# Performance work log

Measured on AMD Instinct MI355X. Metric: run time of the kernel, lower is better.

Reference implementation:

```python
import jax, jax.numpy as jnp
import numpy as np

HIDDEN_DIM = 1024
NUM_EXPERTS = 8
BASE_LR = 0.5
LR_DECAY = 0.85
TOLERANCE = 0.001


def setup_inputs() -> dict:
    key = jax.random.key(0)
    ks = jax.random.split(key, 8)
    B, T, D, E = 4, 2048, HIDDEN_DIM, NUM_EXPERTS
    x_real = jax.random.normal(ks[0], (B, T, D), dtype=jnp.float32)
    x_imag = jax.random.normal(ks[1], (B, T, D), dtype=jnp.float32)
    phase_offset = jax.random.uniform(ks[2], (D,), dtype=jnp.float32) * 2.0 * np.pi
    Wg = jax.random.normal(ks[3], (D, E), dtype=jnp.float32) / np.sqrt(D)
    bg = jnp.zeros((E,), dtype=jnp.float32)
    We = jax.random.normal(ks[4], (E, D, D), dtype=jnp.float32) / np.sqrt(D)
    be = jnp.zeros((E, D), dtype=jnp.float32)
    return {"x_real": x_real, "x_imag": x_imag, "phase_offset": phase_offset,
            "Wg": Wg, "bg": bg, "We": We, "be": be, "local_iterations": 8}


def _moe(z, Wg, bg, We, be, capacity):
    # z: [N, D] complex64. Expert-choice routing on the real part.
    N, D = z.shape
    logits = z.real @ Wg + bg                     # [N, E]
    S = jax.nn.softmax(logits, axis=-1)           # [N, E]
    scores, idx = jax.lax.top_k(S.T, capacity)    # each [E, k]
    gathered = z[idx]                             # [E, k, D] complex
    out_e = jnp.einsum('ekd,edh->ekh', gathered, We.astype(z.dtype)) + be[:, None, :]
    y = jnp.zeros((N, D), z.dtype).at[idx.reshape(-1)].add(
        (scores[..., None] * out_e).reshape(-1, D))
    return y


def _build_target(z, phase_offset):
    # z: [B, T, D] complex; target[t] = z[t-1] * exp(i*phase), target[0] = z[0]
    rot = jnp.exp(1j * phase_offset)              # [D] complex64
    return jnp.concatenate([z[:, :1, :], z[:, :-1, :] * rot], axis=1)


def reference(x_real, x_imag, phase_offset, Wg, bg, We, be, local_iterations):
    B, T, D = x_real.shape
    N = B * T
    capacity = N // NUM_EXPERTS
    z0 = (x_real + 1j * x_imag).astype(jnp.complex64)  # [B, T, D]
    target = _build_target(z0, phase_offset)
    max_iters = max(1, int(local_iterations) - 1)

    def cond(carry):
        it, z, lr, done = carry
        return jnp.logical_and(it < max_iters, jnp.logical_not(done))

    def body(carry):
        it, z, lr, _ = carry
        pred = _moe(z.reshape(N, D), Wg, bg, We, be, capacity).reshape(B, T, D)
        residual = target - pred
        z = z + lr.astype(z.dtype) * residual
        res_mean = jnp.mean(jnp.abs(residual))
        return (it + 1, z, lr * LR_DECAY, res_mean < TOLERANCE)

    it0 = jnp.array(0, jnp.int32)
    lr0 = jnp.array(BASE_LR, jnp.float32)
    iters_run, z_final, _, _ = jax.lax.while_loop(cond, body, (it0, z0, lr0, jnp.array(False)))

    target_grad = _build_target(z0, phase_offset)
    pred_grad = _moe(z_final.reshape(N, D), Wg, bg, We, be, capacity).reshape(B, T, D)
    out = z_final + BASE_LR * (target_grad - pred_grad)   # [B, T, D] complex
    out_stacked = jnp.stack([out.real, out.imag], axis=-1)  # [B, T, D, 2] float32
    return out_stacked, iters_run
```

## Files before the change

kernel.cpp:

```cpp
#include <hip/hip_runtime.h>
#include <math.h>

#define ND    8388608
#define NTOK  8192
#define DIM   1024
#define NEXP  8
#define CAP   1024
#define TSEQ  2048

typedef short bf16x8 __attribute__((ext_vector_type(8)));
typedef unsigned short u16x8 __attribute__((ext_vector_type(8)));
typedef float f32x4 __attribute__((ext_vector_type(4)));

#define AS1 __attribute__((address_space(1)))
#define AS3 __attribute__((address_space(3)))

__device__ __forceinline__ void gload_lds16(const void* g, void* l) {
    __builtin_amdgcn_global_load_lds((const AS1 unsigned int*)g,
                                     (AS3 unsigned int*)l, 16, 0, 0);
}

__device__ __forceinline__ unsigned short f2bf(float x) {
    union { float f; unsigned u; } v; v.f = x;
    unsigned r = v.u + 0x7FFFu + ((v.u >> 16) & 1u);
    return (unsigned short)(r >> 16);
}
__device__ __forceinline__ float bf2f(unsigned short b) {
    union { unsigned u; float f; } v; v.u = ((unsigned)b) << 16; return v.f;
}

__global__ void k_init_small(const float* __restrict__ phase, const int* __restrict__ Lptr,
                             float* __restrict__ rc, float* __restrict__ rs,
                             int* __restrict__ ctl) {
    int d = blockIdx.x * blockDim.x + threadIdx.x;
    if (d < DIM) { rc[d] = cosf(phase[d]); rs[d] = sinf(phase[d]); }
    if (d == 0) {
        ctl[0] = 0; ctl[1] = 0;
        int L = Lptr[0]; int mi = L - 1; if (mi < 1) mi = 1;
        ctl[2] = mi;
    }
}

__global__ void k_init_big(const float* __restrict__ xr, const float* __restrict__ xi,
                           float* __restrict__ zre, unsigned short* __restrict__ zimB) {
    int i = blockIdx.x * blockDim.x + threadIdx.x;
    if (i >= ND) return;
    zre[i] = xr[i];
    zimB[i] = f2bf(xi[i]);
}

__global__ __launch_bounds__(256) void k_wconv(const float* __restrict__ We,
                                               unsigned short* __restrict__ Whi,
                                               unsigned short* __restrict__ Wlo) {
    __shared__ float lds[64][65];
    int e = blockIdx.z, h0 = blockIdx.x * 64, d0 = blockIdx.y * 64;
    int tid = threadIdx.x;
    #pragma unroll
    for (int q = 0; q < 16; ++q) {
        int idx = q * 256 + tid;
        int i = idx >> 6, j = idx & 63;
        lds[i][j] = We[(size_t)e * 1048576 + (size_t)(d0 + i) * 1024 + h0 + j];
    }
    __syncthreads();
    #pragma unroll
    for (int q = 0; q < 2; ++q) {
        int sid = q * 256 + tid;
        int j = sid >> 3, sp = sid & 7;
        int h = h0 + j;
        int slog = sp ^ (h & 7);
        u16x8 hi, lo;
        #pragma unroll
        for (int u = 0; u < 8; ++u) {
            float x = lds[slog * 8 + u][j];
            unsigned short hb = f2bf(x);
            hi[u] = hb;
            lo[u] = f2bf(x - bf2f(hb));
        }
        size_t o = (((size_t)(e << 10) + h) << 10) + d0 + sp * 8;
        *(u16x8*)(Whi + o) = hi;
        *(u16x8*)(Wlo + o) = lo;
    }
}

__global__ __launch_bounds__(256) void k_gate(
    const float* __restrict__ zre, const float* __restrict__ Wg, const float* __restrict__ bg,
    float* __restrict__ S, int* __restrict__ tokcnt,
    const int* __restrict__ ctl, int iter) {
    if (iter >= 0 && (ctl[0] || iter >= ctl[2])) return;
    const int w = threadIdx.x >> 6, lane = threadIdx.x & 63;
    const int n = blockIdx.x * 4 + w;
    const float* zr = zre + ((size_t)n << 10);
    float acc[8] = {0,0,0,0,0,0,0,0};
    #pragma unroll
    for (int q = 0; q < 4; ++q) {
        const int d0 = q * 256 + lane * 4;
        float4 zv = *(const float4*)(zr + d0);
        float zz[4] = {zv.x, zv.y, zv.z, zv.w};
        #pragma unroll
        for (int j = 0; j < 4; ++j) {
            const float4 w0 = *(const float4*)(Wg + (d0 + j) * 8);
            const float4 w1 = *(const float4*)(Wg + (d0 + j) * 8 + 4);
            acc[0] += zz[j] * w0.x; acc[1] += zz[j] * w0.y; acc[2] += zz[j] * w0.z; acc[3] += zz[j] * w0.w;
            acc[4] += zz[j] * w1.x; acc[5] += zz[j] * w1.y; acc[6] += zz[j] * w1.z; acc[7] += zz[j] * w1.w;
        }
    }
    #pragma unroll
    for (int off = 32; off > 0; off >>= 1)
        #pragma unroll
        for (int e = 0; e < 8; ++e) acc[e] += __shfl_xor(acc[e], off);
    if (lane == 0) {
        float m = -1e30f;
        #pragma unroll
        for (int e = 0; e < 8; ++e) { acc[e] += bg[e]; m = fmaxf(m, acc[e]); }
        float sum = 0.f;
        #pragma unroll
        for (int e = 0; e < 8; ++e) { acc[e] = expf(acc[e] - m); sum += acc[e]; }
        float inv = 1.0f / sum;
        *(float4*)(S + (n << 3))     = (float4){acc[0]*inv, acc[1]*inv, acc[2]*inv, acc[3]*inv};
        *(float4*)(S + (n << 3) + 4) = (float4){acc[4]*inv, acc[5]*inv, acc[6]*inv, acc[7]*inv};
        tokcnt[n] = 0;
    }
}

__global__ __launch_bounds__(1024) void k_route(
    const float* __restrict__ S, int* __restrict__ idxs, int* __restrict__ tokcnt,
    int* __restrict__ ent_id, const int* __restrict__ ctl, int iter) {
    if (iter >= 0 && (ctl[0] || iter >= ctl[2])) return;
    __shared__ unsigned keys[NTOK];
    __shared__ unsigned hA[2048];
    __shared__ unsigned hB[2048];
    __shared__ int sbkt, srem, sntie, scnt;
    const int e = blockIdx.x, tid = threadIdx.x;
    if (tid == 0) scnt = 0;
    for (int n = tid; n < NTOK; n += 1024) keys[n] = __float_as_uint(S[(n << 3) + e]);
    __syncthreads();

    int rem = CAP;
    unsigned pref = 0;
    #pragma unroll
    for (int lvl = 0; lvl < 3; ++lvl) {
        const int nb = (lvl == 2) ? 1024 : 2048;
        for (int i = tid; i < nb; i += 1024) hA[i] = 0;
        __syncthreads();
        for (int n = tid; n < NTOK; n += 1024) {
            unsigned k = keys[n];
            bool ok; unsigned b;
            if (lvl == 0)      { ok = true;                 b = k >> 21; }
            else if (lvl == 1) { ok = (k >> 21) == pref;    b = (k >> 10) & 2047u; }
            else               { ok = (k >> 10) == pref;    b = k & 1023u; }
            if (ok) atomicAdd(&hA[b], 1u);
        }
        __syncthreads();
        unsigned* src = hA; unsigned* dst = hB;
        for (int off = 1; off < nb; off <<= 1) {
            for (int i = tid; i < nb; i += 1024)
                dst[i] = src[i] + ((i + off < nb) ? src[i + off] : 0u);
            __syncthreads();
            unsigned* t = src; src = dst; dst = t;
        }
        for (int i = tid; i < nb; i += 1024) {
            unsigned sfi = src[i];
            unsigned sfn = (i + 1 < nb) ? src[i + 1] : 0u;
            if (sfi >= (unsigned)rem && sfn < (unsigned)rem) {
                sbkt = i; srem = rem - (int)sfn; sntie = (int)(sfi - sfn);
            }
        }
        __syncthreads();
        int b = sbkt; rem = srem;
        if (lvl == 0)      pref = (unsigned)b;
        else if (lvl == 1) pref = (pref << 11) | (unsigned)b;
        else               pref = (pref << 10) | (unsigned)b;
        __syncthreads();
    }
    const unsigned T = pref;
    const int remv = rem;
    const bool allt = (remv == sntie);

    for (int n = tid; n < NTOK; n += 1024) {
        unsigned k = keys[n];
        bool sel = (k > T);
        if (k == T) {
            if (allt) sel = true;
            else {
                int r = 0;
                int j = 0;
                for (; j + 8 <= n; j += 8) {
                    r += (int)(keys[j] == T) + (int)(keys[j+1] == T) + (int)(keys[j+2] == T)
                       + (int)(keys[j+3] == T) + (int)(keys[j+4] == T) + (int)(keys[j+5] == T)
                       + (int)(keys[j+6] == T) + (int)(keys[j+7] == T);
                }
                for (; j < n; ++j) r += (int)(keys[j] == T);
                sel = (r < remv);
            }
        }
        if (sel) {
            int slot = atomicAdd(&scnt, 1);
            int row = (e << 10) + slot;
            idxs[row] = n;
            int p = atomicAdd(&tokcnt[n], 1);
            ent_id[(n << 3) + p] = row;
        }
    }
}

__global__ __launch_bounds__(256, 2) void k_gemm_cx(
    const float* __restrict__ zre, const unsigned short* __restrict__ zimB,
    const unsigned short* __restrict__ Whi, const unsigned short* __restrict__ Wlo,
    const float* __restrict__ be, const int* __restrict__ idxs,
    float* __restrict__ outre, float* __restrict__ outim,
    const int* __restrict__ ctl, int iter) {
    if (iter >= 0 && (ctl[0] || iter >= ctl[2])) return;
    extern __shared__ unsigned short smem[];
    const int bid = blockIdx.x;
    const int e = bid & 7, bx = (bid >> 3) & 7, by = bid >> 6;
    const int tid = threadIdx.x;
    const int wid = tid >> 6, lane = tid & 63;
    const int wm = wid >> 1, wn = wid & 1;

    const unsigned short* gsrc = nullptr;
    unsigned short* ldst = nullptr;
    if (wid >= 2) {
        const unsigned short* wsb = (wid == 2) ? Whi : Wlo;
        int rowbase = (e << 10) + bx * 128;
        gsrc = wsb + (((size_t)(rowbase + (lane >> 3))) << 10) + ((lane & 7) << 3);
        ldst = smem + ((wid == 2) ? 24576 : 32768);
    }

    const int rl = lane >> 3;
    const int ch = lane & 7;
    const int slog8 = (ch ^ rl) << 3;
    int tok[4];
    #pragma unroll
    for (int q = 0; q < 4; ++q)
        tok[q] = idxs[(e << 10) + by * 128 + (wid << 5) + (q << 3) + rl];

    f32x4 accre[4][4], accim[4][4];
    #pragma unroll
    for (int a = 0; a < 4; ++a)
        #pragma unroll
        for (int b = 0; b < 4; ++b) {
            accre[a][b] = (f32x4){0.f, 0.f, 0.f, 0.f};
            accim[a][b] = (f32x4){0.f, 0.f, 0.f, 0.f};
        }

    for (int kt = 0; kt < DIM; kt += 64) {
        if (kt) __syncthreads();
        if (wid >= 2) {
            #pragma unroll
            for (int i = 0; i < 16; ++i)
                gload_lds16(gsrc + kt + ((size_t)i << 13), ldst + i * 512);
        }
        float4 a0[4], a1[4]; u16x8 im[4];
        #pragma unroll
        for (int q = 0; q < 4; ++q) {
            const float* zsrc = zre + ((size_t)tok[q] << 10) + kt + slog8;
            a0[q] = *(const float4*)zsrc;
            a1[q] = *(const float4*)(zsrc + 4);
            im[q] = *(const u16x8*)(zimB + ((size_t)tok[q] << 10) + kt + slog8);
        }
        #pragma unroll
        for (int q = 0; q < 4; ++q) {
            const int r = (wid << 5) + (q << 3) + rl;
            const int lo_off = (r << 6) + (ch << 3);
            float xv[8] = {a0[q].x, a0[q].y, a0[q].z, a0[q].w,
                           a1[q].x, a1[q].y, a1[q].z, a1[q].w};
            u16x8 hi, lo;
            #pragma unroll
            for (int u = 0; u < 8; ++u) {
                unsigned short hb = f2bf(xv[u]);
                hi[u] = hb;
                lo[u] = f2bf(xv[u] - bf2f(hb));
            }
            *(u16x8*)&smem[lo_off]         = hi;
            *(u16x8*)&smem[8192 + lo_off]  = lo;
            *(u16x8*)&smem[16384 + lo_off] = im[q];
        }
        __syncthreads();
        #pragma unroll
        for (int ks = 0; ks < 2; ++ks) {
            const int slog = (ks << 2) + (lane >> 4);
            const int swz = (slog ^ (lane & 7)) << 3;
            bf16x8 ah[4], al[4], am[4], bh[4], bl[4];
            #pragma unroll
            for (int mi = 0; mi < 4; ++mi) {
                int off = ((wm * 64 + mi * 16 + (lane & 15)) << 6) + swz;
                ah[mi] = *(const bf16x8*)&smem[off];
                al[mi] = *(const bf16x8*)&smem[8192 + off];
                am[mi] = *(const bf16x8*)&smem[16384 + off];
            }
            #pragma unroll
            for (int ni = 0; ni < 4; ++ni) {
                int off = ((wn * 64 + ni * 16 + (lane & 15)) << 6) + swz;
                bh[ni] = *(const bf16x8*)&smem[24576 + off];
                bl[ni] = *(const bf16x8*)&smem[32768 + off];
            }
            #pragma unroll
            for (int mi = 0; mi < 4; ++mi)
                #pragma unroll
                for (int ni = 0; ni < 4; ++ni) {
                    accre[mi][ni] = __builtin_amdgcn_mfma_f32_16x16x32_bf16(ah[mi], bh[ni], accre[mi][ni], 0, 0, 0);
                    accre[mi][ni] = __builtin_amdgcn_mfma_f32_16x16x32_bf16(ah[mi], bl[ni], accre[mi][ni], 0, 0, 0);
                    accre[mi][ni] = __builtin_amdgcn_mfma_f32_16x16x32_bf16(al[mi], bh[ni], accre[mi][ni], 0, 0, 0);
                    accim[mi][ni] = __builtin_amdgcn_mfma_f32_16x16x32_bf16(am[mi], bh[ni], accim[mi][ni], 0, 0, 0);
                }
        }
    }
    const int colbase = bx * 128 + wn * 64 + (lane & 15);
    float bev[4];
    #pragma unroll
    for (int ni = 0; ni < 4; ++ni) bev[ni] = be[(e << 10) + colbase + ni * 16];
    const int rowloc = by * 128 + wm * 64 + ((lane >> 4) << 2);
    float* obr = outre + (((size_t)(e << 10) + rowloc) << 10) + colbase;
    float* obi = outim + (((size_t)(e << 10) + rowloc) << 10) + colbase;
    #pragma unroll
    for (int mi = 0; mi < 4; ++mi)
        #pragma unroll
        for (int rg = 0; rg < 4; ++rg) {
            size_t ro = (size_t)(mi * 16 + rg) << 10;
            #pragma unroll
            for (int ni = 0; ni < 4; ++ni) {
                obr[ro + ni * 16] = accre[mi][ni][rg] + bev[ni];
                obi[ro + ni * 16] = accim[mi][ni][rg];
            }
        }
}

__global__ __launch_bounds__(256) void k_resid_gate(
    float* __restrict__ zre, unsigned short* __restrict__ zimB,
    const float* __restrict__ xr, const float* __restrict__ xi,
    const float* __restrict__ rc, const float* __restrict__ rs,
    const float* __restrict__ outre, const float* __restrict__ outim,
    int* __restrict__ tokcnt, const int* __restrict__ ent_id,
    float* __restrict__ S, const float* __restrict__ Wg, const float* __restrict__ bg,
    float lr, float* __restrict__ partial, const int* __restrict__ ctl, int iter) {
    if (ctl[0] || iter >= ctl[2]) return;
    __shared__ float wred[4][8];
    const int n = blockIdx.x;
    const int tid = threadIdx.x;
    const int d0 = tid << 2;
    const int kc = tokcnt[n];
    const int4 e0 = *(const int4*)(ent_id + (n << 3));
    const int4 e1 = *(const int4*)(ent_id + (n << 3) + 4);
    const int rows[8] = {e0.x, e0.y, e0.z, e0.w, e1.x, e1.y, e1.z, e1.w};

    float pr[4] = {0,0,0,0}, pm[4] = {0,0,0,0};
    #pragma unroll
    for (int k = 0; k < 8; ++k) {
        if (k < kc) {
            const int row = rows[k];
            const float s = S[(n << 3) + (row >> 10)];
            const float4 vr = *(const float4*)(outre + ((size_t)row << 10) + d0);
            const float4 vi = *(const float4*)(outim + ((size_t)row << 10) + d0);
            pr[0] += s * vr.x; pr[1] += s * vr.y; pr[2] += s * vr.z; pr[3] += s * vr.w;
            pm[0] += s * vi.x; pm[1] += s * vi.y; pm[2] += s * vi.z; pm[3] += s * vi.w;
        }
    }
    const size_t base = ((size_t)n << 10) + d0;
    const int t = n & (TSEQ - 1);
    float tr[4], ti[4];
    if (t == 0) {
        float4 a = *(const float4*)(xr + base), b = *(const float4*)(xi + base);
        tr[0]=a.x; tr[1]=a.y; tr[2]=a.z; tr[3]=a.w;
        ti[0]=b.x; ti[1]=b.y; ti[2]=b.z; ti[3]=b.w;
    } else {
        float4 a = *(const float4*)(xr + base - DIM), b = *(const float4*)(xi + base - DIM);
        float4 c = *(const float4*)(rc + d0), s4 = *(const float4*)(rs + d0);
        tr[0]=a.x*c.x-b.x*s4.x; tr[1]=a.y*c.y-b.y*s4.y; tr[2]=a.z*c.z-b.z*s4.z; tr[3]=a.w*c.w-b.w*s4.w;
        ti[0]=a.x*s4.x+b.x*c.x; ti[1]=a.y*s4.y+b.y*c.y; ti[2]=a.z*s4.z+b.z*c.z; ti[3]=a.w*s4.w+b.w*c.w;
    }
    float4 zr4 = *(const float4*)(zre + base);
    ushort4 zi4 = *(const ushort4*)(zimB + base);
    float zrv[4] = {zr4.x, zr4.y, zr4.z, zr4.w};
    unsigned short ziv[4] = {zi4.x, zi4.y, zi4.z, zi4.w};
    float zn[4]; unsigned short zo[4];
    float lsum = 0.f;
    float lac[8] = {0,0,0,0,0,0,0,0};
    #pragma unroll
    for (int j = 0; j < 4; ++j) {
        float rr = tr[j] - pr[j];
        float ri = ti[j] - pm[j];
        zn[j] = zrv[j] + lr * rr;
        zo[j] = f2bf(bf2f(ziv[j]) + lr * ri);
        lsum += sqrtf(rr * rr + ri * ri);
        const float4 w0 = *(const float4*)(Wg + (d0 + j) * 8);
        const float4 w1 = *(const float4*)(Wg + (d0 + j) * 8 + 4);
        lac[0] += zn[j] * w0.x; lac[1] += zn[j] * w0.y; lac[2] += zn[j] * w0.z; lac[3] += zn[j] * w0.w;
        lac[4] += zn[j] * w1.x; lac[5] += zn[j] * w1.y; lac[6] += zn[j] * w1.z; lac[7] += zn[j] * w1.w;
    }
    *(float4*)(zre + base) = (float4){zn[0], zn[1], zn[2], zn[3]};
    *(ushort4*)(zimB + base) = (ushort4){zo[0], zo[1], zo[2], zo[3]};

    const int w = tid >> 6, lane = tid & 63;
    #pragma unroll
    for (int off = 32; off > 0; off >>= 1) {
        lsum += __shfl_xor(lsum, off);
        #pragma unroll
        for (int e = 0; e < 8; ++e) lac[e] += __shfl_xor(lac[e], off);
    }
    if (lane == 0) {
        #pragma unroll
        for (int e = 0; e < 8; ++e) wred[w][e] = lac[e];
        partial[(n << 2) + w] = lsum;
    }
    __syncthreads();
    if (tid == 0) {
        float lg[8];
        float m = -1e30f;
        #pragma unroll
        for (int e = 0; e < 8; ++e) {
            lg[e] = wred[0][e] + wred[1][e] + wred[2][e] + wred[3][e] + bg[e];
            m = fmaxf(m, lg[e]);
        }
        float sum = 0.f;
        #pragma unroll
        for (int e = 0; e < 8; ++e) { lg[e] = expf(lg[e] - m); sum += lg[e]; }
        float inv = 1.0f / sum;
        *(float4*)(S + (n << 3))     = (float4){lg[0]*inv, lg[1]*inv, lg[2]*inv, lg[3]*inv};
        *(float4*)(S + (n << 3) + 4) = (float4){lg[4]*inv, lg[5]*inv, lg[6]*inv, lg[7]*inv};
        tokcnt[n] = 0;
    }
}

__global__ __launch_bounds__(1024) void k_finalize(
    const float* __restrict__ partial, int* __restrict__ ctl, int iter) {
    if (ctl[0] || iter >= ctl[2]) return;
    __shared__ float red[16];
    float s = 0.f;
    for (int i = threadIdx.x; i < NTOK * 4; i += 1024) s += partial[i];
    #pragma unroll
    for (int off = 32; off > 0; off >>= 1) s += __shfl_xor(s, off);
    if ((threadIdx.x & 63) == 0) red[threadIdx.x >> 6] = s;
    __syncthreads();
    if (threadIdx.x == 0) {
        float tot = 0.f;
        #pragma unroll
        for (int w = 0; w < 16; ++w) tot += red[w];
        ctl[1] = iter + 1;
        if (tot * (1.0f / (float)ND) < 0.001f) ctl[0] = 1;
    }
}

__global__ __launch_bounds__(256) void k_final_zupd(
    float* __restrict__ zre, unsigned short* __restrict__ zimB,
    const float* __restrict__ xr, const float* __restrict__ xi,
    const float* __restrict__ rc, const float* __restrict__ rs,
    const float* __restrict__ outre, const float* __restrict__ outim,
    const int* __restrict__ tokcnt, const int* __restrict__ ent_id,
    const float* __restrict__ S) {
    const int n = blockIdx.x;
    const int tid = threadIdx.x;
    const int d0 = tid << 2;
    const int kc = tokcnt[n];
    const int4 e0 = *(const int4*)(ent_id + (n << 3));
    const int4 e1 = *(const int4*)(ent_id + (n << 3) + 4);
    const int rows[8] = {e0.x, e0.y, e0.z, e0.w, e1.x, e1.y, e1.z, e1.w};
    float pr[4] = {0,0,0,0}, pm[4] = {0,0,0,0};
    #pragma unroll
    for (int k = 0; k < 8; ++k) {
        if (k < kc) {
            const int row = rows[k];
            const float s = S[(n << 3) + (row >> 10)];
            const float4 vr = *(const float4*)(outre + ((size_t)row << 10) + d0);
            const float4 vi = *(const float4*)(outim + ((size_t)row << 10) + d0);
            pr[0] += s * vr.x; pr[1] += s * vr.y; pr[2] += s * vr.z; pr[3] += s * vr.w;
            pm[0] += s * vi.x; pm[1] += s * vi.y; pm[2] += s * vi.z; pm[3] += s * vi.w;
        }
    }
    const size_t base = ((size_t)n << 10) + d0;
    const int t = n & (TSEQ - 1);
    float tr[4], ti[4];
    if (t == 0) {
        float4 a = *(const float4*)(xr + base), b = *(const float4*)(xi + base);
        tr[0]=a.x; tr[1]=a.y; tr[2]=a.z; tr[3]=a.w;
        ti[0]=b.x; ti[1]=b.y; ti[2]=b.z; ti[3]=b.w;
    } else {
        float4 a = *(const float4*)(xr + base - DIM), b = *(const float4*)(xi + base - DIM);
        float4 c = *(const float4*)(rc + d0), s4 = *(const float4*)(rs + d0);
        tr[0]=a.x*c.x-b.x*s4.x; tr[1]=a.y*c.y-b.y*s4.y; tr[2]=a.z*c.z-b.z*s4.z; tr[3]=a.w*c.w-b.w*s4.w;
        ti[0]=a.x*s4.x+b.x*c.x; ti[1]=a.y*s4.y+b.y*c.y; ti[2]=a.z*s4.z+b.z*c.z; ti[3]=a.w*s4.w+b.w*c.w;
    }
    float4 zr4 = *(const float4*)(zre + base);
    ushort4 zi4 = *(const ushort4*)(zimB + base);
    float zrv[4] = {zr4.x, zr4.y, zr4.z, zr4.w};
    unsigned short ziv[4] = {zi4.x, zi4.y, zi4.z, zi4.w};
    float zn[4]; unsigned short zo[4];
    #pragma unroll
    for (int j = 0; j < 4; ++j) {
        zn[j] = zrv[j] + 0.5f * (tr[j] - pr[j]);
        zo[j] = f2bf(bf2f(ziv[j]) + 0.5f * (ti[j] - pm[j]));
    }
    *(float4*)(zre + base) = (float4){zn[0], zn[1], zn[2], zn[3]};
    *(ushort4*)(zimB + base) = (ushort4){zo[0], zo[1], zo[2], zo[3]};
}

__global__ void k_write_out(const float* __restrict__ zre, const unsigned short* __restrict__ zimB,
                            float* __restrict__ out, const int* __restrict__ ctl) {
    int i = blockIdx.x * blockDim.x + threadIdx.x;
    if (i >= ND) return;
    out[2 * i]     = zre[i];
    out[2 * i + 1] = bf2f(zimB[i]);
    if (i == 0) out[(size_t)2 * ND] = (float)ctl[1];
}

extern "C" void kernel_launch(void* const* d_in, const int* in_sizes, int n_in,
                              void* d_out, int out_size, void* d_ws, size_t ws_size,
                              hipStream_t stream) {
    (void)in_sizes; (void)n_in; (void)out_size; (void)ws_size;
    const float* x_real = (const float*)d_in[0];
    const float* x_imag = (const float*)d_in[1];
    const float* phase  = (const float*)d_in[2];
    const float* Wg     = (const float*)d_in[3];
    const float* bg     = (const float*)d_in[4];
    const float* We     = (const float*)d_in[5];
    const float* be     = (const float*)d_in[6];
    const int*   Lptr   = (const int*)d_in[7];

    char* wsb = (char*)d_ws;
    float*          zre  = (float*)wsb;
    unsigned short* zimB = (unsigned short*)(wsb + 33554432);
    unsigned short* Whi  = (unsigned short*)(wsb + 50331648);
    unsigned short* Wlo  = (unsigned short*)(wsb + 67108864);
    float*    S       = (float*)(wsb + 83886080);
    int*      ent_id  = (int*)  (wsb + 84148224);
    int*      idxs    = (int*)  (wsb + 84410368);
    int*      tokcnt  = (int*)  (wsb + 84443136);
    float*    partial = (float*)(wsb + 84475904);
    float*    rc      = (float*)(wsb + 84606976);
    float*    rs      = (float*)(wsb + 84611072);
    int*      ctl     = (int*)  (wsb + 84615168);

    float* outre = (float*)d_out;
    float* outim = outre + (size_t)ND;

    k_init_small<<<4, 256, 0, stream>>>(phase, Lptr, rc, rs, ctl);
    k_init_big<<<ND / 256, 256, 0, stream>>>(x_real, x_imag, zre, zimB);
    k_wconv<<<dim3(16, 16, 8), 256, 0, stream>>>(We, Whi, Wlo);
    k_gate<<<NTOK / 4, 256, 0, stream>>>(zre, Wg, bg, S, tokcnt, ctl, -1);

    const size_t gemm_lds = 40960 * sizeof(unsigned short);
    float lr = 0.5f;
    for (int it = 0; it < 7; ++it) {
        k_route<<<NEXP, 1024, 0, stream>>>(S, idxs, tokcnt, ent_id, ctl, it);
        k_gemm_cx<<<512, 256, gemm_lds, stream>>>(zre, zimB, Whi, Wlo, be, idxs,
                                                  outre, outim, ctl, it);
        k_resid_gate<<<NTOK, 256, 0, stream>>>(zre, zimB, x_real, x_imag, rc, rs,
                                               outre, outim, tokcnt, ent_id, S, Wg, bg,
                                               lr, partial, ctl, it);
        k_finalize<<<1, 1024, 0, stream>>>(partial, ctl, it);
        lr *= 0.85f;
    }

    k_route<<<NEXP, 1024, 0, stream>>>(S, idxs, tokcnt, ent_id, ctl, -1);
    k_gemm_cx<<<512, 256, gemm_lds, stream>>>(zre, zimB, Whi, Wlo, be, idxs,
                                              outre, outim, ctl, -1);
    k_final_zupd<<<NTOK, 256, 0, stream>>>(zre, zimB, x_real, x_imag, rc, rs,
                                           outre, outim, tokcnt, ent_id, S);
    k_write_out<<<ND / 256, 256, 0, stream>>>(zre, zimB, (float*)d_out, ctl);
}
```

Before: 1.239 ms.

## Store real state as split bf16 hi/lo planes and DMA gathered rows into LDS

The real part of z is now stored as two bf16 planes (hi and lo) instead of fp32, and the split is done by the producer kernels (init, residual update) rather than inside the GEMM. The GEMM then gathers token rows straight into LDS with global_load_lds from three warps, while the fourth warp and partial slices handle the weight tiles. This drops the per-tile fp32 load, convert and LDS store from the GEMM inner loop, and merges init_big into the gate kernel. In exchange, every z update re-splits into hi/lo and the real state keeps only about bf16+bf16 precision, so rounding can drift slightly across iterations.

After: 1.160 ms. -6.4%, faster.

```diff
diff --git a/kernel.cpp b/kernel.cpp
--- a/kernel.cpp
+++ b/kernel.cpp
@@ -41,14 +41,6 @@
     }
 }
 
-__global__ void k_init_big(const float* __restrict__ xr, const float* __restrict__ xi,
-                           float* __restrict__ zre, unsigned short* __restrict__ zimB) {
-    int i = blockIdx.x * blockDim.x + threadIdx.x;
-    if (i >= ND) return;
-    zre[i] = xr[i];
-    zimB[i] = f2bf(xi[i]);
-}
-
 __global__ __launch_bounds__(256) void k_wconv(const float* __restrict__ We,
                                                unsigned short* __restrict__ Whi,
                                                unsigned short* __restrict__ Wlo) {
@@ -82,27 +74,38 @@
     }
 }
 
-__global__ __launch_bounds__(256) void k_gate(
-    const float* __restrict__ zre, const float* __restrict__ Wg, const float* __restrict__ bg,
-    float* __restrict__ S, int* __restrict__ tokcnt,
-    const int* __restrict__ ctl, int iter) {
-    if (iter >= 0 && (ctl[0] || iter >= ctl[2])) return;
+__global__ __launch_bounds__(256) void k_init_gate(
+    const float* __restrict__ xr, const float* __restrict__ xi,
+    unsigned short* __restrict__ zhi, unsigned short* __restrict__ zlo,
+    unsigned short* __restrict__ zimB,
+    const float* __restrict__ Wg, const float* __restrict__ bg,
+    float* __restrict__ S, int* __restrict__ tokcnt) {
     const int w = threadIdx.x >> 6, lane = threadIdx.x & 63;
     const int n = blockIdx.x * 4 + w;
-    const float* zr = zre + ((size_t)n << 10);
     float acc[8] = {0,0,0,0,0,0,0,0};
     #pragma unroll
     for (int q = 0; q < 4; ++q) {
         const int d0 = q * 256 + lane * 4;
-        float4 zv = *(const float4*)(zr + d0);
-        float zz[4] = {zv.x, zv.y, zv.z, zv.w};
+        const size_t base = ((size_t)n << 10) + d0;
+        float4 xv = *(const float4*)(xr + base);
+        float4 iv = *(const float4*)(xi + base);
+        float zz[4] = {xv.x, xv.y, xv.z, xv.w};
+        float zi[4] = {iv.x, iv.y, iv.z, iv.w};
+        unsigned short h4[4], l4[4], i4[4];
         #pragma unroll
         for (int j = 0; j < 4; ++j) {
+            unsigned short hb = f2bf(zz[j]);
+            h4[j] = hb;
+            l4[j] = f2bf(zz[j] - bf2f(hb));
+            i4[j] = f2bf(zi[j]);
             const float4 w0 = *(const float4*)(Wg + (d0 + j) * 8);
             const float4 w1 = *(const float4*)(Wg + (d0 + j) * 8 + 4);
             acc[0] += zz[j] * w0.x; acc[1] += zz[j] * w0.y; acc[2] += zz[j] * w0.z; acc[3] += zz[j] * w0.w;
             acc[4] += zz[j] * w1.x; acc[5] += zz[j] * w1.y; acc[6] += zz[j] * w1.z; acc[7] += zz[j] * w1.w;
         }
+        *(ushort4*)(zhi + base)  = (ushort4){h4[0], h4[1], h4[2], h4[3]};
+        *(ushort4*)(zlo + base)  = (ushort4){l4[0], l4[1], l4[2], l4[3]};
+        *(ushort4*)(zimB + base) = (ushort4){i4[0], i4[1], i4[2], i4[3]};
     }
     #pragma unroll
     for (int off = 32; off > 0; off >>= 1)
@@ -204,7 +207,8 @@
 }
 
 __global__ __launch_bounds__(256, 2) void k_gemm_cx(
-    const float* __restrict__ zre, const unsigned short* __restrict__ zimB,
+    const unsigned short* __restrict__ zhi, const unsigned short* __restrict__ zlo,
+    const unsigned short* __restrict__ zimB,
     const unsigned short* __restrict__ Whi, const unsigned short* __restrict__ Wlo,
     const float* __restrict__ be, const int* __restrict__ idxs,
     float* __restrict__ outre, float* __restrict__ outim,
@@ -216,23 +220,21 @@
     const int tid = threadIdx.x;
     const int wid = tid >> 6, lane = tid & 63;
     const int wm = wid >> 1, wn = wid & 1;
-
-    const unsigned short* gsrc = nullptr;
-    unsigned short* ldst = nullptr;
-    if (wid >= 2) {
-        const unsigned short* wsb = (wid == 2) ? Whi : Wlo;
-        int rowbase = (e << 10) + bx * 128;
-        gsrc = wsb + (((size_t)(rowbase + (lane >> 3))) << 10) + ((lane & 7) << 3);
-        ldst = smem + ((wid == 2) ? 24576 : 32768);
-    }
-
-    const int rl = lane >> 3;
-    const int ch = lane & 7;
-    const int slog8 = (ch ^ rl) << 3;
-    int tok[4];
-    #pragma unroll
-    for (int q = 0; q < 4; ++q)
-        tok[q] = idxs[(e << 10) + by * 128 + (wid << 5) + (q << 3) + rl];
+    const int rl = lane >> 3, ch = lane & 7;
+    const int swz8 = (ch ^ rl) << 3;
+
+    int tok[16];
+    if (wid < 3) {
+        #pragma unroll
+        for (int c = 0; c < 16; ++c)
+            tok[c] = idxs[(e << 10) + by * 128 + c * 8 + rl];
+    }
+    const unsigned short* aplane = (wid == 0) ? zhi : (wid == 1) ? zlo : zimB;
+    unsigned short* albase = smem + (wid << 13);
+
+    const int wrowbase = (e << 10) + bx * 128;
+    const unsigned short* whsrc = Whi + (((size_t)(wrowbase + rl)) << 10) + (ch << 3);
+    const unsigned short* wlsrc = Wlo + (((size_t)(wrowbase + rl)) << 10) + (ch << 3);
 
     f32x4 accre[4][4], accim[4][4];
     #pragma unroll
@@ -245,35 +247,19 @@
 
     for (int kt = 0; kt < DIM; kt += 64) {
         if (kt) __syncthreads();
-        if (wid >= 2) {
+        if (wid < 3) {
             #pragma unroll
-            for (int i = 0; i < 16; ++i)
-                gload_lds16(gsrc + kt + ((size_t)i << 13), ldst + i * 512);
-        }
-        float4 a0[4], a1[4]; u16x8 im[4];
+            for (int c = 0; c < 16; ++c)
+                gload_lds16(aplane + (((size_t)tok[c]) << 10) + kt + swz8, albase + c * 512);
+        } else {
+            #pragma unroll
+            for (int c = 0; c < 16; ++c)
+                gload_lds16(whsrc + kt + ((size_t)c << 13), smem + 24576 + c * 512);
+        }
         #pragma unroll
         for (int q = 0; q < 4; ++q) {
-            const float* zsrc = zre + ((size_t)tok[q] << 10) + kt + slog8;
-            a0[q] = *(const float4*)zsrc;
-            a1[q] = *(const float4*)(zsrc + 4);
-            im[q] = *(const u16x8*)(zimB + ((size_t)tok[q] << 10) + kt + slog8);
-        }
-        #pragma unroll
-        for (int q = 0; q < 4; ++q) {
-            const int r = (wid << 5) + (q << 3) + rl;
-            const int lo_off = (r << 6) + (ch << 3);
-            float xv[8] = {a0[q].x, a0[q].y, a0[q].z, a0[q].w,
-                           a1[q].x, a1[q].y, a1[q].z, a1[q].w};
-            u16x8 hi, lo;
-            #pragma unroll
-            for (int u = 0; u < 8; ++u) {
-                unsigned short hb = f2bf(xv[u]);
-                hi[u] = hb;
-                lo[u] = f2bf(xv[u] - bf2f(hb));
-            }
-            *(u16x8*)&smem[lo_off]         = hi;
-            *(u16x8*)&smem[8192 + lo_off]  = lo;
-            *(u16x8*)&smem[16384 + lo_off] = im[q];
+            int c = (wid << 2) + q;
+            gload_lds16(wlsrc + kt + ((size_t)c << 13), smem + 32768 + c * 512);
         }
         __syncthreads();
         #pragma unroll
@@ -326,7 +312,8 @@
 }
 
 __global__ __launch_bounds__(256) void k_resid_gate(
-    float* __restrict__ zre, unsigned short* __restrict__ zimB,
+    unsigned short* __restrict__ zhi, unsigned short* __restrict__ zlo,
+    unsigned short* __restrict__ zimB,
     const float* __restrict__ xr, const float* __restrict__ xi,
     const float* __restrict__ rc, const float* __restrict__ rs,
     const float* __restrict__ outre, const float* __restrict__ outim,
@@ -368,26 +355,32 @@
         tr[0]=a.x*c.x-b.x*s4.x; tr[1]=a.y*c.y-b.y*s4.y; tr[2]=a.z*c.z-b.z*s4.z; tr[3]=a.w*c.w-b.w*s4.w;
         ti[0]=a.x*s4.x+b.x*c.x; ti[1]=a.y*s4.y+b.y*c.y; ti[2]=a.z*s4.z+b.z*c.z; ti[3]=a.w*s4.w+b.w*c.w;
     }
-    float4 zr4 = *(const float4*)(zre + base);
+    ushort4 h4 = *(const ushort4*)(zhi + base);
+    ushort4 l4 = *(const ushort4*)(zlo + base);
     ushort4 zi4 = *(const ushort4*)(zimB + base);
-    float zrv[4] = {zr4.x, zr4.y, zr4.z, zr4.w};
+    float zrv[4] = {bf2f(h4.x)+bf2f(l4.x), bf2f(h4.y)+bf2f(l4.y),
+                    bf2f(h4.z)+bf2f(l4.z), bf2f(h4.w)+bf2f(l4.w)};
     unsigned short ziv[4] = {zi4.x, zi4.y, zi4.z, zi4.w};
-    float zn[4]; unsigned short zo[4];
+    unsigned short hn[4], ln[4], zo[4];
     float lsum = 0.f;
     float lac[8] = {0,0,0,0,0,0,0,0};
     #pragma unroll
     for (int j = 0; j < 4; ++j) {
         float rr = tr[j] - pr[j];
         float ri = ti[j] - pm[j];
-        zn[j] = zrv[j] + lr * rr;
+        float zn = zrv[j] + lr * rr;
+        unsigned short hb = f2bf(zn);
+        hn[j] = hb;
+        ln[j] = f2bf(zn - bf2f(hb));
         zo[j] = f2bf(bf2f(ziv[j]) + lr * ri);
         lsum += sqrtf(rr * rr + ri * ri);
         const float4 w0 = *(const float4*)(Wg + (d0 + j) * 8);
         const float4 w1 = *(const float4*)(Wg + (d0 + j) * 8 + 4);
-        lac[0] += zn[j] * w0.x; lac[1] += zn[j] * w0.y; lac[2] += zn[j] * w0.z; lac[3] += zn[j] * w0.w;
-        lac[4] += zn[j] * w1.x; lac[5] += zn[j] * w1.y; lac[6] += zn[j] * w1.z; lac[7] += zn[j] * w1.w;
-    }
-    *(float4*)(zre + base) = (float4){zn[0], zn[1], zn[2], zn[3]};
+        lac[0] += zn * w0.x; lac[1] += zn * w0.y; lac[2] += zn * w0.z; lac[3] += zn * w0.w;
+        lac[4] += zn * w1.x; lac[5] += zn * w1.y; lac[6] += zn * w1.z; lac[7] += zn * w1.w;
+    }
+    *(ushort4*)(zhi + base)  = (ushort4){hn[0], hn[1], hn[2], hn[3]};
+    *(ushort4*)(zlo + base)  = (ushort4){ln[0], ln[1], ln[2], ln[3]};
     *(ushort4*)(zimB + base) = (ushort4){zo[0], zo[1], zo[2], zo[3]};
 
     const int w = tid >> 6, lane = tid & 63;
@@ -441,7 +434,8 @@
 }
 
 __global__ __launch_bounds__(256) void k_final_zupd(
-    float* __restrict__ zre, unsigned short* __restrict__ zimB,
+    unsigned short* __restrict__ zhi, unsigned short* __restrict__ zlo,
+    unsigned short* __restrict__ zimB,
     const float* __restrict__ xr, const float* __restrict__ xi,
     const float* __restrict__ rc, const float* __restrict__ rs,
     const float* __restrict__ outre, const float* __restrict__ outim,
@@ -479,25 +473,33 @@
         tr[0]=a.x*c.x-b.x*s4.x; tr[1]=a.y*c.y-b.y*s4.y; tr[2]=a.z*c.z-b.z*s4.z; tr[3]=a.w*c.w-b.w*s4.w;
         ti[0]=a.x*s4.x+b.x*c.x; ti[1]=a.y*s4.y+b.y*c.y; ti[2]=a.z*s4.z+b.z*c.z; ti[3]=a.w*s4.w+b.w*c.w;
     }
-    float4 zr4 = *(const float4*)(zre + base);
+    ushort4 h4 = *(const ushort4*)(zhi + base);
+    ushort4 l4 = *(const ushort4*)(zlo + base);
     ushort4 zi4 = *(const ushort4*)(zimB + base);
-    float zrv[4] = {zr4.x, zr4.y, zr4.z, zr4.w};
+    float zrv[4] = {bf2f(h4.x)+bf2f(l4.x), bf2f(h4.y)+bf2f(l4.y),
+                    bf2f(h4.z)+bf2f(l4.z), bf2f(h4.w)+bf2f(l4.w)};
     unsigned short ziv[4] = {zi4.x, zi4.y, zi4.z, zi4.w};
-    float zn[4]; unsigned short zo[4];
+    unsigned short hn[4], ln[4], zo[4];
     #pragma unroll
     for (int j = 0; j < 4; ++j) {
-        zn[j] = zrv[j] + 0.5f * (tr[j] - pr[j]);
+        float zn = zrv[j] + 0.5f * (tr[j] - pr[j]);
+        unsigned short hb = f2bf(zn);
+        hn[j] = hb;
+        ln[j] = f2bf(zn - bf2f(hb));
         zo[j] = f2bf(bf2f(ziv[j]) + 0.5f * (ti[j] - pm[j]));
     }
-    *(float4*)(zre + base) = (float4){zn[0], zn[1], zn[2], zn[3]};
+    *(ushort4*)(zhi + base)  = (ushort4){hn[0], hn[1], hn[2], hn[3]};
+    *(ushort4*)(zlo + base)  = (ushort4){ln[0], ln[1], ln[2], ln[3]};
     *(ushort4*)(zimB + base) = (ushort4){zo[0], zo[1], zo[2], zo[3]};
 }
 
-__global__ void k_write_out(const float* __restrict__ zre, const unsigned short* __restrict__ zimB,
+__global__ void k_write_out(const unsigned short* __restrict__ zhi,
+                            const unsigned short* __restrict__ zlo,
+                            const unsigned short* __restrict__ zimB,
                             float* __restrict__ out, const int* __restrict__ ctl) {
     int i = blockIdx.x * blockDim.x + threadIdx.x;
     if (i >= ND) return;
-    out[2 * i]     = zre[i];
+    out[2 * i]     = bf2f(zhi[i]) + bf2f(zlo[i]);
     out[2 * i + 1] = bf2f(zimB[i]);
     if (i == 0) out[(size_t)2 * ND] = (float)ctl[1];
 }
@@ -516,7 +518,8 @@
     const int*   Lptr   = (const int*)d_in[7];
 
     char* wsb = (char*)d_ws;
-    float*          zre  = (float*)wsb;
+    unsigned short* zhi  = (unsigned short*)wsb;
+    unsigned short* zlo  = (unsigned short*)(wsb + 16777216);
     unsigned short* zimB = (unsigned short*)(wsb + 33554432);
     unsigned short* Whi  = (unsigned short*)(wsb + 50331648);
     unsigned short* Wlo  = (unsigned short*)(wsb + 67108864);
@@ -533,17 +536,16 @@
     float* outim = outre + (size_t)ND;
 
     k_init_small<<<4, 256, 0, stream>>>(phase, Lptr, rc, rs, ctl);
-    k_init_big<<<ND / 256, 256, 0, stream>>>(x_real, x_imag, zre, zimB);
     k_wconv<<<dim3(16, 16, 8), 256, 0, stream>>>(We, Whi, Wlo);
-    k_gate<<<NTOK / 4, 256, 0, stream>>>(zre, Wg, bg, S, tokcnt, ctl, -1);
+    k_init_gate<<<NTOK / 4, 256, 0, stream>>>(x_real, x_imag, zhi, zlo, zimB, Wg, bg, S, tokcnt);
 
     const size_t gemm_lds = 40960 * sizeof(unsigned short);
     float lr = 0.5f;
     for (int it = 0; it < 7; ++it) {
         k_route<<<NEXP, 1024, 0, stream>>>(S, idxs, tokcnt, ent_id, ctl, it);
-        k_gemm_cx<<<512, 256, gemm_lds, stream>>>(zre, zimB, Whi, Wlo, be, idxs,
+        k_gemm_cx<<<512, 256, gemm_lds, stream>>>(zhi, zlo, zimB, Whi, Wlo, be, idxs,
                                                   outre, outim, ctl, it);
-        k_resid_gate<<<NTOK, 256, 0, stream>>>(zre, zimB, x_real, x_imag, rc, rs,
+        k_resid_gate<<<NTOK, 256, 0, stream>>>(zhi, zlo, zimB, x_real, x_imag, rc, rs,
                                                outre, outim, tokcnt, ent_id, S, Wg, bg,
                                                lr, partial, ctl, it);
         k_finalize<<<1, 1024, 0, stream>>>(partial, ctl, it);
@@ -551,9 +553,9 @@
     }
 
     k_route<<<NEXP, 1024, 0, stream>>>(S, idxs, tokcnt, ent_id, ctl, -1);
-    k_gemm_cx<<<512, 256, gemm_lds, stream>>>(zre, zimB, Whi, Wlo, be, idxs,
+    k_gemm_cx<<<512, 256, gemm_lds, stream>>>(zhi, zlo, zimB, Whi, Wlo, be, idxs,
                                               outre, outim, ctl, -1);
-    k_final_zupd<<<NTOK, 256, 0, stream>>>(zre, zimB, x_real, x_imag, rc, rs,
+    k_final_zupd<<<NTOK, 256, 0, stream>>>(zhi, zlo, zimB, x_real, x_imag, rc, rs,
                                            outre, outim, tokcnt, ent_id, S);
-    k_write_out<<<ND / 256, 256, 0, stream>>>(zre, zimB, (float*)d_out, ctl);
-}
+    k_write_out<<<ND / 256, 256, 0, stream>>>(zhi, zlo, zimB, (float*)d_out, ctl);
+}
```
